# Kernel optimization log

Measured on AMD Instinct MI355X. Metric: run time of the kernel, lower is better.

## Reference

```python
import jax, jax.numpy as jnp
import numpy as np
from jax import lax

NUM_CLASSES = 80
CONF = 0.05
IOU_T = 0.5
K_PER_CLASS = 100   # max_detections_per_class
MAX_DET = 100       # max_detections
BOX_VAR = np.array([0.1, 0.1, 0.2, 0.2], dtype=np.float32)


def make_anchors(H, W):
    """AnchorBox.get_anchors: [x, y, w, h] anchors for strides 8..128."""
    ratios = [0.5, 1.0, 2.0]
    scales = [2.0 ** 0, 2.0 ** (1.0 / 3.0), 2.0 ** (2.0 / 3.0)]
    strides = [8, 16, 32, 64, 128]
    areas = [32.0 ** 2, 64.0 ** 2, 128.0 ** 2, 256.0 ** 2, 512.0 ** 2]
    out = []
    for stride, area in zip(strides, areas):
        fh = int(np.ceil(H / stride)); fw = int(np.ceil(W / stride))
        dims = []
        for r in ratios:
            ah = np.sqrt(area / r); aw = area / ah
            for s in scales:
                dims.append([aw * s, ah * s])
        dims = np.array(dims, dtype=np.float32)              # [9,2]
        rx = (np.arange(fw, dtype=np.float32) + 0.5) * stride
        ry = (np.arange(fh, dtype=np.float32) + 0.5) * stride
        cx, cy = np.meshgrid(rx, ry)                         # [fh,fw]
        centers = np.stack([cx, cy], axis=-1)                # [fh,fw,2]
        centers = np.tile(centers[:, :, None, :], (1, 1, 9, 1))
        d = np.tile(dims[None, None, :, :], (fh, fw, 1, 1))
        out.append(np.concatenate([centers, d], axis=-1).reshape(-1, 4))
    return np.concatenate(out, axis=0).astype(np.float32)   # [N,4]


def _iou_matrix(boxes):
    # boxes: [K,4] corner format (x1,y1,x2,y2)
    lt = jnp.maximum(boxes[:, None, :2], boxes[None, :, :2])
    rb = jnp.minimum(boxes[:, None, 2:], boxes[None, :, 2:])
    inter = jnp.prod(jnp.clip(rb - lt, 0.0), axis=-1)
    area = jnp.prod(boxes[:, 2:] - boxes[:, :2], axis=-1)
    union = area[:, None] + area[None, :] - inter
    return inter / jnp.maximum(union, 1e-8)


def _decode(predictions, anchors):
    box_pred = predictions[..., :4] * jnp.asarray(BOX_VAR)
    xy = box_pred[..., :2] * anchors[:, 2:] + anchors[:, :2]
    wh = jnp.exp(box_pred[..., 2:]) * anchors[:, 2:]
    boxes = jnp.concatenate([xy - wh / 2.0, xy + wh / 2.0], axis=-1)  # [B,N,4] corners
    cls = jax.nn.sigmoid(predictions[..., 4:])                        # [B,N,C]
    return boxes, cls


def _nms_image(boxes, cls_scores):
    # boxes [N,4], cls_scores [N,C]
    rng = jnp.arange(K_PER_CLASS)

    def per_class(scores):  # [N]
        top_s, idx = lax.top_k(scores, K_PER_CLASS)
        cb = boxes[idx]                                      # [K,4]
        iou = lax.stop_gradient(_iou_matrix(cb))
        keep0 = top_s > CONF
        def body(i, keep):
            sup = keep[i] & (iou[i] > IOU_T) & (rng > i)
            return keep & (~sup)
        keep = lax.fori_loop(0, K_PER_CLASS, body, keep0)
        return cb, jnp.where(keep, top_s, -1.0)

    cboxes, cscores = jax.vmap(per_class)(cls_scores.T)      # [C,K,4], [C,K]
    cids = jnp.broadcast_to(jnp.arange(NUM_CLASSES, dtype=jnp.float32)[:, None],
                            (NUM_CLASSES, K_PER_CLASS))
    flat_s = cscores.reshape(-1)
    flat_b = cboxes.reshape(-1, 4)
    flat_c = cids.reshape(-1)
    fs, fi = lax.top_k(flat_s, MAX_DET)
    fb = flat_b[fi]
    fc = flat_c[fi]
    mask = fs > 0.0
    valid = jnp.sum(mask).astype(jnp.int32)
    return (jnp.where(mask[:, None], fb, 0.0),
            jnp.where(mask, fs, 0.0),
            jnp.where(mask, fc, 0.0),
            valid)


def setup_inputs() -> dict:
    key = jax.random.key(0)
    k1, k2 = jax.random.split(key)
    images = jax.random.normal(k1, (8, 512, 512, 3), dtype=jnp.float32)
    predictions = jax.random.normal(k2, (8, 49104, 84), dtype=jnp.float32)
    return {"images": images, "predictions": predictions}


def reference(images, predictions):
    H, W = images.shape[1], images.shape[2]
    anchors = jnp.asarray(make_anchors(H, W))                # [49104,4]
    boxes, cls = _decode(predictions, anchors)
    nmsed_boxes, nmsed_scores, nmsed_classes, valid = jax.vmap(_nms_image)(boxes, cls)
    return nmsed_boxes, nmsed_scores, nmsed_classes, valid
```

## Files before the change

### kernel.cpp

```cpp
#include <hip/hip_runtime.h>
#include <math.h>
#include <stdint.h>

#define NANCH 49104
#define NCLS 80
#define KSEL 100
#define NFLAT (NCLS * KSEL)
#define PREDC 84
#define NB 8
#define ECAP 128
#define BATF4 (NANCH * (PREDC / 4))
#define BPB 256
#define PCAP 16
#define LCAP 16
#define OCAP 64
#define FASTN 512
#define RMAX 8
#define CGRP 5
#define NCHUNK (NCLS / CGRP)
#define THRL 2.5f

struct DimsTable { float d[5][9][2]; };
struct KT { uint32_t key; int tie; };
typedef unsigned long long u64;

__device__ __forceinline__ uint32_t f2key(float f) {
    uint32_t u = __float_as_uint(f);
    return u ^ (uint32_t((int32_t)u >> 31) | 0x80000000u);
}
__device__ __forceinline__ float key2f(uint32_t k) {
    uint32_t u = (k & 0x80000000u) ? (k ^ 0x80000000u) : ~k;
    return __uint_as_float(u);
}
__device__ __forceinline__ float sigm(float x) { return 1.0f / (1.0f + expf(-x)); }

__device__ __forceinline__ void decode_box(const float4 pv, int n,
                                           const DimsTable& dt, float box[4]) {
    int lev, base, fw, stride;
    if (n < 36864)      { lev = 0; base = 0;     fw = 64; stride = 8;   }
    else if (n < 46080) { lev = 1; base = 36864; fw = 32; stride = 16;  }
    else if (n < 48384) { lev = 2; base = 46080; fw = 16; stride = 32;  }
    else if (n < 48960) { lev = 3; base = 48384; fw = 8;  stride = 64;  }
    else                { lev = 4; base = 48960; fw = 4;  stride = 128; }
    int i = n - base;
    int k = i % 9;
    int cell = i / 9;
    int xq = cell % fw, yq = cell / fw;
    float cx = ((float)xq + 0.5f) * (float)stride;
    float cy = ((float)yq + 0.5f) * (float)stride;
    float aw = dt.d[lev][k][0];
    float ah = dt.d[lev][k][1];
    float tx = __fmul_rn(pv.x, 0.1f);
    float ty = __fmul_rn(pv.y, 0.1f);
    float tw = __fmul_rn(pv.z, 0.2f);
    float th = __fmul_rn(pv.w, 0.2f);
    float px = __fadd_rn(__fmul_rn(tx, aw), cx);
    float py = __fadd_rn(__fmul_rn(ty, ah), cy);
    float pw = __fmul_rn(expf(tw), aw);
    float ph = __fmul_rn(expf(th), ah);
    float hw = __fmul_rn(pw, 0.5f);
    float hh = __fmul_rn(ph, 0.5f);
    box[0] = __fsub_rn(px, hw);
    box[1] = __fsub_rn(py, hh);
    box[2] = __fadd_rn(px, hw);
    box[3] = __fadd_rn(py, hh);
}

struct alignas(16) SelSh {
    int hist[2048];
    int suffix[256];
    uint32_t candKey[KSEL];
    int candIdx[KSEL];
    uint32_t eIdx[ECAP];
    uint32_t sKey[KSEL];
    int sIdx[KSEL];
    int cntG, cntE, krem, newkrem, digit, flast, rmin;
    uint32_t prefix, thrKey;
};

template <typename G>
__device__ int block_select(G get, int N, int K, SelSh& sh) {
    const int tid = threadIdx.x;
    int Ksel = (N < K) ? N : K;
    if (Ksel <= 0) return 0;

    if (N <= K) {
        if (tid < N) { KT e = get(tid); sh.candKey[tid] = e.key; sh.candIdx[tid] = e.tie; }
        __syncthreads();
        if (tid < N) {
            uint32_t mk = sh.candKey[tid]; int mi = sh.candIdx[tid];
            int rank = 0;
            for (int j = 0; j < N; ++j) {
                uint32_t kj = sh.candKey[j]; int ij = sh.candIdx[j];
                rank += (kj > mk) || (kj == mk && ij < mi);
            }
            sh.sKey[rank] = mk; sh.sIdx[rank] = mi;
        }
        __syncthreads();
        return Ksel;
    }

    if (tid == 0) { sh.krem = K; sh.prefix = 0; }
    for (int pass = 0; pass < 3; ++pass) {
        const int bins   = (pass == 2) ? 1024 : 2048;
        const int dshift = (pass == 0) ? 21 : (pass == 1 ? 10 : 0);
        const int fshift = (pass == 1) ? 21 : 10;
        const int dmask  = bins - 1;
        for (int j = tid; j < bins; j += 256) sh.hist[j] = 0;
        __syncthreads();
        const uint32_t pref = sh.prefix;
        for (int i = tid; i < N; i += 256) {
            uint32_t key = get(i).key;
            if (pass == 0) {
                atomicAdd(&sh.hist[(key >> dshift) & dmask], 1);
            } else if ((key >> fshift) == pref) {
                atomicAdd(&sh.hist[(key >> dshift) & dmask], 1);
            }
        }
        __syncthreads();
        const int cpb = bins / 256;
        const int base = tid * cpb;
        int lsum = 0;
        for (int j = 0; j < cpb; ++j) lsum += sh.hist[base + j];
        sh.suffix[tid] = lsum;
        __syncthreads();
        for (int off = 1; off < 256; off <<= 1) {
            int v = (tid + off < 256) ? sh.suffix[tid + off] : 0;
            __syncthreads();
            sh.suffix[tid] += v;
            __syncthreads();
        }
        {
            int cum = sh.suffix[tid] - lsum;
            const int krem = sh.krem;
            for (int j = cpb - 1; j >= 0; --j) {
                int cnt = sh.hist[base + j];
                if (cnt > 0 && cum < krem && cum + cnt >= krem) {
                    sh.digit = base + j;
                    sh.newkrem = krem - cum;
                }
                cum += cnt;
            }
        }
        __syncthreads();
        if (tid == 0) {
            sh.krem = sh.newkrem;
            if (pass == 0)      sh.prefix = (uint32_t)sh.digit;
            else if (pass == 1) sh.prefix = (sh.prefix << 11) | (uint32_t)sh.digit;
            else                sh.thrKey = (sh.prefix << 10) | (uint32_t)sh.digit;
        }
        __syncthreads();
    }

    if (tid == 0) { sh.cntG = 0; sh.cntE = 0; }
    __syncthreads();
    const uint32_t thr = sh.thrKey;
    for (int i = tid; i < N; i += 256) {
        KT e = get(i);
        if (e.key > thr) {
            int g = atomicAdd(&sh.cntG, 1);
            sh.candKey[g] = e.key; sh.candIdx[g] = e.tie;
        } else if (e.key == thr) {
            int idx = atomicAdd(&sh.cntE, 1);
            if (idx < ECAP) sh.eIdx[idx] = (uint32_t)e.tie;
        }
    }
    __syncthreads();
    const int need = sh.krem;
    const int nG = K - need;
    if (sh.cntE <= ECAP) {
        const int ce = sh.cntE;
        if (tid < ce) {
            uint32_t my = sh.eIdx[tid];
            int rank = 0;
            for (int j = 0; j < ce; ++j) rank += (sh.eIdx[j] < my);
            if (rank < need) { sh.candKey[nG + rank] = thr; sh.candIdx[nG + rank] = (int)my; }
        }
    } else {
        if (tid == 0) sh.flast = -1;
        __syncthreads();
        for (int t = 0; t < need; ++t) {
            if (tid == 0) sh.rmin = 0x7FFFFFFF;
            __syncthreads();
            const int fl = sh.flast;
            int lmin = 0x7FFFFFFF;
            for (int i = tid; i < N; i += 256) {
                KT e = get(i);
                if (e.key == thr && e.tie > fl) lmin = min(lmin, e.tie);
            }
            atomicMin(&sh.rmin, lmin);
            __syncthreads();
            if (tid == 0) { sh.candKey[nG + t] = thr; sh.candIdx[nG + t] = sh.rmin; sh.flast = sh.rmin; }
            __syncthreads();
        }
    }
    __syncthreads();
    if (tid < K) {
        uint32_t mk = sh.candKey[tid]; int mi = sh.candIdx[tid];
        int rank = 0;
        for (int j = 0; j < K; ++j) {
            uint32_t kj = sh.candKey[j]; int ij = sh.candIdx[j];
            rank += (kj > mk) || (kj == mk && ij < mi);
        }
        sh.sKey[rank] = mk; sh.sIdx[rank] = mi;
    }
    __syncthreads();
    return Ksel;
}

__global__ __launch_bounds__(256) void init_k(int* __restrict__ oflowCnt) {
    for (int x = threadIdx.x; x < NB * NCLS; x += 256) oflowCnt[x] = 0;
}

__device__ __forceinline__ void procf4(float4 p, int v, int b,
                                       int* lcnt, uint2 (*buck)[LCAP],
                                       int* oflowCnt, uint2* oflow) {
    uint32_t q = (uint32_t)v / 21u;
    uint32_t j = (uint32_t)v - q * 21u;
    if (j == 0u) return;
    bool c0 = p.x > THRL, c1 = p.y > THRL, c2 = p.z > THRL, c3 = p.w > THRL;
    if (!(c0 | c1 | c2 | c3)) return;
    uint32_t row = q - (uint32_t)b * (uint32_t)NANCH;
    int cbase = ((int)j - 1) * 4;
    float vv[4] = {p.x, p.y, p.z, p.w};
    bool pp[4] = {c0, c1, c2, c3};
#pragma unroll
    for (int k = 0; k < 4; ++k) {
        if (pp[k]) {
            int c = cbase + k;
            uint32_t key = f2key(sigm(vv[k]));
            int slot = atomicAdd(&lcnt[c], 1);
            if (slot < LCAP) {
                buck[c][slot] = make_uint2(key, row);
            } else {
                int bc = b * NCLS + c;
                int gs = atomicAdd(&oflowCnt[bc], 1);
                if (gs < OCAP) oflow[(size_t)bc * OCAP + gs] = make_uint2(key, row);
            }
        }
    }
}

__global__ __launch_bounds__(256) void cand_scan(const float4* __restrict__ predv,
                                                 uint2* __restrict__ cand2,
                                                 int* __restrict__ cnt2,
                                                 int* __restrict__ oflowCnt,
                                                 uint2* __restrict__ oflow) {
    __shared__ uint2 buck[NCLS][LCAP];
    __shared__ int lcnt[NCLS];

    const int tid = threadIdx.x;
    const int b = blockIdx.x / BPB;
    const int part = blockIdx.x - b * BPB;
    const int CH = (BATF4 + BPB - 1) / BPB;

    for (int j = tid; j < NCLS; j += 256) lcnt[j] = 0;
    __syncthreads();

    int s = b * BATF4 + part * CH;
    int e = b * BATF4 + BATF4;
    if (s + CH < e) e = s + CH;

    int v = s + tid;
    for (; v + 7 * 256 < e; v += 8 * 256) {
        float4 a0 = predv[v];
        float4 a1 = predv[v + 1 * 256];
        float4 a2 = predv[v + 2 * 256];
        float4 a3 = predv[v + 3 * 256];
        float4 a4 = predv[v + 4 * 256];
        float4 a5 = predv[v + 5 * 256];
        float4 a6 = predv[v + 6 * 256];
        float4 a7 = predv[v + 7 * 256];
        procf4(a0, v,           b, lcnt, buck, oflowCnt, oflow);
        procf4(a1, v + 1 * 256, b, lcnt, buck, oflowCnt, oflow);
        procf4(a2, v + 2 * 256, b, lcnt, buck, oflowCnt, oflow);
        procf4(a3, v + 3 * 256, b, lcnt, buck, oflowCnt, oflow);
        procf4(a4, v + 4 * 256, b, lcnt, buck, oflowCnt, oflow);
        procf4(a5, v + 5 * 256, b, lcnt, buck, oflowCnt, oflow);
        procf4(a6, v + 6 * 256, b, lcnt, buck, oflowCnt, oflow);
        procf4(a7, v + 7 * 256, b, lcnt, buck, oflowCnt, oflow);
    }
    for (; v < e; v += 256)
        procf4(predv[v], v, b, lcnt, buck, oflowCnt, oflow);
    __syncthreads();

    if (tid < NCLS) {
        int lc = lcnt[tid];
        if (lc > LCAP) lc = LCAP;
        cnt2[((size_t)b * NCLS + tid) * BPB + part] = lc;
    }
    for (int x = tid; x < NCLS * LCAP; x += 256) {
        int c = x >> 4;
        int k = x & (LCAP - 1);
        int lc = lcnt[c];
        if (lc > LCAP) lc = LCAP;
        if (k < lc)
            cand2[((size_t)(b * NCLS + c) * PCAP + k) * BPB + part] = buck[c][k];
    }
}

__global__ __launch_bounds__(256) void nms_sel(const float* __restrict__ pred,
                                               const uint2* __restrict__ cand2,
                                               const int* __restrict__ cnt2,
                                               const int* __restrict__ oflowCnt,
                                               const uint2* __restrict__ oflow,
                                               float* __restrict__ cls_boxes,
                                               uint32_t* __restrict__ posKeyC,
                                               uint32_t* __restrict__ posFlatC,
                                               int* __restrict__ posCntC,
                                               DimsTable dt) {
    __shared__ SelSh sh;
    __shared__ uint16_t prank[4][FASTN];
    __shared__ int wtot[4];
    __shared__ float sbox[KSEL][4];
    __shared__ float sarea[KSEL];
    __shared__ int sconf[KSEL];
    __shared__ alignas(16) uint32_t sup[KSEL][4];
    __shared__ uint32_t keepm[4];
    const int c = blockIdx.x;
    const int b = blockIdx.y;
    const int tid = threadIdx.x;
    const int bc = b * NCLS + c;
    const int lane = tid & 63;
    const int wid = tid >> 6;

    int myc = cnt2[(size_t)bc * BPB + tid];
    {
        int x = myc;
        for (int off = 1; off < 64; off <<= 1) {
            int y = __shfl_up(x, off);
            if (lane >= off) x += y;
        }
        if (lane == 63) wtot[wid] = x;
        __syncthreads();
        int base = 0;
#pragma unroll
        for (int w = 0; w < 4; ++w) if (w < wid) base += wtot[w];
        sh.suffix[tid] = base + x - myc;
    }
    const int excl = sh.suffix[tid];
    const int n0 = wtot[0] + wtot[1] + wtot[2] + wtot[3];
    const int of = oflowCnt[bc];
    const int n = n0 + of;

    if (n >= KSEL && n <= FASTN && of <= OCAP) {
        u64* list64 = (u64*)sh.hist;
        for (int k = 0; k < myc; ++k) {
            uint2 p = cand2[((size_t)bc * PCAP + k) * BPB + tid];
            list64[excl + k] = ((u64)p.x << 32) | (u64)(~p.y);
        }
        for (int x = tid; x < of; x += 256) {
            uint2 p = oflow[(size_t)bc * OCAP + x];
            list64[n0 + x] = ((u64)p.x << 32) | (u64)(~p.y);
        }
        __syncthreads();
        u64 cl[RMAX];
        int pr[RMAX];
#pragma unroll
        for (int r = 0; r < RMAX; ++r) {
            int i = r * 64 + lane;
            cl[r] = (i < n) ? list64[i] : 0xFFFFFFFFFFFFFFFFull;
            pr[r] = 0;
        }
        const int js = (wid * n) >> 2;
        const int je = ((wid + 1) * n) >> 2;
        int j = js;
        for (; j + 3 < je; j += 4) {
            u64 o0 = list64[j];
            u64 o1 = list64[j + 1];
            u64 o2 = list64[j + 2];
            u64 o3 = list64[j + 3];
#pragma unroll
            for (int r = 0; r < RMAX; ++r)
                pr[r] += (o0 > cl[r]) + (o1 > cl[r]) + (o2 > cl[r]) + (o3 > cl[r]);
        }
        for (; j < je; ++j) {
            u64 o = list64[j];
#pragma unroll
            for (int r = 0; r < RMAX; ++r) pr[r] += (o > cl[r]);
        }
#pragma unroll
        for (int r = 0; r < RMAX; ++r) {
            int i = r * 64 + lane;
            if (i < n) prank[wid][i] = (uint16_t)pr[r];
        }
        __syncthreads();
        for (int i = tid; i < n; i += 256) {
            int rank = (int)prank[0][i] + (int)prank[1][i]
                     + (int)prank[2][i] + (int)prank[3][i];
            if (rank < KSEL) {
                u64 e = list64[i];
                sh.sKey[rank] = (uint32_t)(e >> 32);
                sh.sIdx[rank] = (int)(~(uint32_t)e);
            }
        }
        __syncthreads();
    } else {
        const float* src = pred + (size_t)b * NANCH * PREDC + 4 + c;
        auto g = [src](int i) { KT e; e.key = f2key(sigm(src[(size_t)i * PREDC])); e.tie = i; return e; };
        block_select(g, NANCH, KSEL, sh);
    }

    for (int x = tid; x < KSEL * 4; x += 256) ((uint32_t*)sup)[x] = 0;
    if (tid < KSEL) {
        int ni = sh.sIdx[tid];
        float4 pv = reinterpret_cast<const float4*>(pred)[((size_t)b * NANCH + ni) * (PREDC / 4)];
        float bx[4]; decode_box(pv, ni, dt, bx);
        sbox[tid][0] = bx[0]; sbox[tid][1] = bx[1];
        sbox[tid][2] = bx[2]; sbox[tid][3] = bx[3];
        sarea[tid] = __fmul_rn(__fsub_rn(bx[2], bx[0]), __fsub_rn(bx[3], bx[1]));
        sconf[tid] = (key2f(sh.sKey[tid]) > 0.05f) ? 1 : 0;
    }
    __syncthreads();

    for (int pidx = tid; pidx < KSEL * KSEL; pidx += 256) {
        int i = pidx / KSEL;
        int jj = pidx - i * KSEL;
        if (jj > i && sconf[i] && sconf[jj]) {
            float x1 = fmaxf(sbox[i][0], sbox[jj][0]);
            float y1 = fmaxf(sbox[i][1], sbox[jj][1]);
            float x2 = fminf(sbox[i][2], sbox[jj][2]);
            float y2 = fminf(sbox[i][3], sbox[jj][3]);
            float iw = fmaxf(__fsub_rn(x2, x1), 0.0f);
            float ih = fmaxf(__fsub_rn(y2, y1), 0.0f);
            float inter = __fmul_rn(iw, ih);
            float uni = __fsub_rn(__fadd_rn(sarea[i], sarea[jj]), inter);
            if (__fdiv_rn(inter, fmaxf(uni, 1e-8f)) > 0.5f)
                atomicOr(&sup[i][jj >> 5], 1u << (jj & 31));
        }
    }
    __syncthreads();

    if (tid < 64) {
        const int l = tid;
        uint4 rowA = *reinterpret_cast<const uint4*>(sup[l]);
        int confA = sconf[l];
        uint4 rowB = make_uint4(0u, 0u, 0u, 0u);
        int confB = 0;
        if (l + 64 < KSEL) {
            rowB = *reinterpret_cast<const uint4*>(sup[l + 64]);
            confB = sconf[l + 64];
        }
        u64 mA = __ballot(confA != 0);
        u64 mB = __ballot(confB != 0);
        uint32_t k0 = (uint32_t)mA, k1 = (uint32_t)(mA >> 32);
        uint32_t k2 = (uint32_t)mB, k3 = (uint32_t)(mB >> 32);
        for (int i = 0; i < KSEL; ++i) {
            uint32_t w = (i < 32) ? k0 : (i < 64) ? k1 : (i < 96) ? k2 : k3;
            if ((w >> (i & 31)) & 1u) {
                uint32_t s0, s1, s2, s3;
                if (i < 64) {
                    s0 = __shfl(rowA.x, i); s1 = __shfl(rowA.y, i);
                    s2 = __shfl(rowA.z, i); s3 = __shfl(rowA.w, i);
                } else {
                    s0 = __shfl(rowB.x, i - 64); s1 = __shfl(rowB.y, i - 64);
                    s2 = __shfl(rowB.z, i - 64); s3 = __shfl(rowB.w, i - 64);
                }
                k0 &= ~s0; k1 &= ~s1; k2 &= ~s2; k3 &= ~s3;
            }
        }
        if (l == 0) {
            keepm[0] = k0; keepm[1] = k1; keepm[2] = k2; keepm[3] = k3;
            posCntC[bc] = __popc(k0) + __popc(k1) + __popc(k2) + __popc(k3);
        }
    }
    __syncthreads();

    if (tid < KSEL) {
        reinterpret_cast<float4*>(cls_boxes)[(size_t)b * NFLAT + c * KSEL + tid] =
            make_float4(sbox[tid][0], sbox[tid][1], sbox[tid][2], sbox[tid][3]);
        int w = tid >> 5, bit = tid & 31;
        if ((keepm[w] >> bit) & 1u) {
            int off = __popc(keepm[w] & ((bit == 0) ? 0u : ((1u << bit) - 1u)));
            for (int ww = 0; ww < w; ++ww) off += __popc(keepm[ww]);
            posKeyC[(size_t)bc * KSEL + off] = sh.sKey[tid];
            posFlatC[(size_t)bc * KSEL + off] = (uint32_t)(c * KSEL + tid);
        }
    }
}

__global__ __launch_bounds__(256) void chunk_sel(const uint32_t* __restrict__ posKeyC,
                                                 const uint32_t* __restrict__ posFlatC,
                                                 const int* __restrict__ posCntC,
                                                 u64* __restrict__ chunkOut,
                                                 int* __restrict__ chunkN) {
    __shared__ u64 list64[FASTN];
    __shared__ uint16_t prank[4][FASTN];
    __shared__ int csh[CGRP + 1];
    __shared__ u64 osel[KSEL];
    const int g = blockIdx.x;
    const int b = blockIdx.y;
    const int tid = threadIdx.x;
    const int lane = tid & 63;
    const int wid = tid >> 6;
    const int c0 = g * CGRP;

    if (tid == 0) {
        int acc = 0;
        for (int cc = 0; cc < CGRP; ++cc) {
            csh[cc] = acc;
            acc += posCntC[b * NCLS + c0 + cc];
        }
        csh[CGRP] = acc;
    }
    __syncthreads();
    const int n = csh[CGRP];

    for (int idx = tid; idx < CGRP * KSEL; idx += 256) {
        int cc = idx / KSEL;
        int k = idx - cc * KSEL;
        int base = csh[cc];
        if (k < csh[cc + 1] - base) {
            size_t sp = (size_t)(b * NCLS + c0 + cc) * KSEL + k;
            list64[base + k] = ((u64)posKeyC[sp] << 32) | (u64)(~posFlatC[sp]);
        }
    }
    __syncthreads();

    if (n > 0) {
        u64 cl[RMAX];
        int pr[RMAX];
#pragma unroll
        for (int r = 0; r < RMAX; ++r) {
            int i = r * 64 + lane;
            cl[r] = (i < n) ? list64[i] : 0xFFFFFFFFFFFFFFFFull;
            pr[r] = 0;
        }
        const int js = (wid * n) >> 2;
        const int je = ((wid + 1) * n) >> 2;
        int j = js;
        for (; j + 3 < je; j += 4) {
            u64 o0 = list64[j];
            u64 o1 = list64[j + 1];
            u64 o2 = list64[j + 2];
            u64 o3 = list64[j + 3];
#pragma unroll
            for (int r = 0; r < RMAX; ++r)
                pr[r] += (o0 > cl[r]) + (o1 > cl[r]) + (o2 > cl[r]) + (o3 > cl[r]);
        }
        for (; j < je; ++j) {
            u64 o = list64[j];
#pragma unroll
            for (int r = 0; r < RMAX; ++r) pr[r] += (o > cl[r]);
        }
#pragma unroll
        for (int r = 0; r < RMAX; ++r) {
            int i = r * 64 + lane;
            if (i < n) prank[wid][i] = (uint16_t)pr[r];
        }
        __syncthreads();
        for (int i = tid; i < n; i += 256) {
            int rank = (int)prank[0][i] + (int)prank[1][i]
                     + (int)prank[2][i] + (int)prank[3][i];
            if (rank < KSEL) osel[rank] = list64[i];
        }
    }
    __syncthreads();
    const int kn = (n < KSEL) ? n : KSEL;
    if (tid < kn)
        chunkOut[(size_t)(b * NCHUNK + g) * KSEL + tid] = osel[tid];
    if (tid == 0) chunkN[b * NCHUNK + g] = kn;
}

__global__ __launch_bounds__(256) void merge_sel(const u64* __restrict__ chunkOut,
                                                 const int* __restrict__ chunkN,
                                                 const float* __restrict__ cls_boxes,
                                                 float* __restrict__ out) {
    __shared__ u64 lst[NCHUNK][KSEL];
    __shared__ int ln[NCHUNK];
    __shared__ u64 osel[KSEL];
    __shared__ int okcnt;
    const int b = blockIdx.x;
    const int tid = threadIdx.x;

    if (tid < NCHUNK) ln[tid] = chunkN[b * NCHUNK + tid];
    if (tid == 0) okcnt = 0;
    __syncthreads();
    for (int x = tid; x < NCHUNK * KSEL; x += 256) {
        int g = x / KSEL;
        int k = x - g * KSEL;
        lst[g][k] = (k < ln[g]) ? chunkOut[(size_t)(b * NCHUNK + g) * KSEL + k] : 0ull;
    }
    __syncthreads();

    if (tid < 64) {
        const int l = tid;
        u64 h = (l < NCHUNK) ? lst[l][0] : 0ull;
        int p = 0;
        for (int r = 0; r < KSEL; ++r) {
            u64 m = h;
#pragma unroll
            for (int off = 8; off >= 1; off >>= 1) {
                u64 o = __shfl_xor(m, off);
                if (o > m) m = o;
            }
            if (l < NCHUNK && h == m && m != 0ull) {
                ++p;
                h = (p < ln[l]) ? lst[l][p] : 0ull;
            }
            if (l == 0) osel[r] = m;
        }
    }
    __syncthreads();

    if (tid < KSEL) {
        u64 e = osel[tid];
        float4 ob = make_float4(0.f, 0.f, 0.f, 0.f);
        float sv = 0.f, cv = 0.f;
        if (e != 0ull) {
            uint32_t key = (uint32_t)(e >> 32);
            int flat = (int)(~(uint32_t)e);
            sv = key2f(key);
            ob = reinterpret_cast<const float4*>(cls_boxes)[(size_t)b * NFLAT + flat];
            cv = (float)(flat / KSEL);
            atomicAdd(&okcnt, 1);
        }
        reinterpret_cast<float4*>(out)[(size_t)b * KSEL + tid] = ob;
        out[NB * KSEL * 4 + b * KSEL + tid] = sv;
        out[NB * KSEL * 5 + b * KSEL + tid] = cv;
    }
    __syncthreads();
    if (tid == 0) out[NB * KSEL * 6 + b] = (float)okcnt;
}

extern "C" void kernel_launch(void* const* d_in, const int* in_sizes, int n_in,
                              void* d_out, int out_size, void* d_ws, size_t ws_size,
                              hipStream_t stream) {
    const float* pred = (const float*)d_in[1];
    float* out = (float*)d_out;

    DimsTable dt;
    const double areasd[5] = {1024.0, 4096.0, 16384.0, 65536.0, 262144.0};
    const double ratios[3] = {0.5, 1.0, 2.0};
    const double scales[3] = {1.0, pow(2.0, 1.0 / 3.0), pow(2.0, 2.0 / 3.0)};
    for (int l = 0; l < 5; ++l)
        for (int ri = 0; ri < 3; ++ri) {
            double ah = sqrt(areasd[l] / ratios[ri]);
            double aw = areasd[l] / ah;
            for (int si = 0; si < 3; ++si) {
                dt.d[l][ri * 3 + si][0] = (float)(aw * scales[si]);
                dt.d[l][ri * 3 + si][1] = (float)(ah * scales[si]);
            }
        }

    char* wsb = (char*)d_ws;
    int* oflowCnt = (int*)wsb;
    int* posCntC  = oflowCnt + NB * NCLS;
    int* chunkNb  = posCntC + NB * NCLS;
    uint2* oflow  = (uint2*)(wsb + 16384);
    uint2* cand2  = oflow + (size_t)NB * NCLS * OCAP;
    int* cnt2     = (int*)(cand2 + (size_t)NB * NCLS * PCAP * BPB);
    float* cls_boxes = (float*)(cnt2 + (size_t)NB * NCLS * BPB);
    uint32_t* posKeyC  = (uint32_t*)(cls_boxes + (size_t)NB * NFLAT * 4);
    uint32_t* posFlatC = posKeyC + (size_t)NB * NFLAT;
    u64* chunkOut = (u64*)(posFlatC + (size_t)NB * NFLAT);

    init_k<<<1, 256, 0, stream>>>(oflowCnt);

    cand_scan<<<NB * BPB, 256, 0, stream>>>(reinterpret_cast<const float4*>(pred),
                                            cand2, cnt2, oflowCnt, oflow);

    dim3 gb(NCLS, NB);
    nms_sel<<<gb, 256, 0, stream>>>(pred, cand2, cnt2, oflowCnt, oflow,
                                    cls_boxes, posKeyC, posFlatC, posCntC, dt);

    dim3 gc(NCHUNK, NB);
    chunk_sel<<<gc, 256, 0, stream>>>(posKeyC, posFlatC, posCntC, chunkOut, chunkNb);

    merge_sel<<<NB, 256, 0, stream>>>(chunkOut, chunkNb, cls_boxes, out);
}
```

Baseline: 118.5 us.

## Fuse chunk selection and merge into a single two-level k-way merge kernel

Replaces the two-kernel top-K pipeline (per-chunk rank-based selection over 16 chunks of 5 classes, then a 16-way merge) with one kernel per image. Each of four wavefronts runs a 20-way heap-head merge over sorted per-class lists using 32-lane shuffles, and a second 4-way merge then picks the final top 100. This removes a kernel launch and the chunkOut round trip through global memory. In exchange, each image is handled by a single block running two serial 100-step merge loops, with 64 KB of shared memory for the lists.

Result: slower. 143.6 us (+21.2%).

```diff
diff --git a/kernel.cpp b/kernel.cpp
--- a/kernel.cpp
+++ b/kernel.cpp
@@ -16,8 +16,6 @@
 #define OCAP 64
 #define FASTN 512
 #define RMAX 8
-#define CGRP 5
-#define NCHUNK (NCLS / CGRP)
 #define THRL 2.5f
 
 struct DimsTable { float d[5][9][2]; };
@@ -479,126 +477,70 @@
     }
 }
 
-__global__ __launch_bounds__(256) void chunk_sel(const uint32_t* __restrict__ posKeyC,
-                                                 const uint32_t* __restrict__ posFlatC,
-                                                 const int* __restrict__ posCntC,
-                                                 u64* __restrict__ chunkOut,
-                                                 int* __restrict__ chunkN) {
-    __shared__ u64 list64[FASTN];
-    __shared__ uint16_t prank[4][FASTN];
-    __shared__ int csh[CGRP + 1];
-    __shared__ u64 osel[KSEL];
-    const int g = blockIdx.x;
-    const int b = blockIdx.y;
-    const int tid = threadIdx.x;
-    const int lane = tid & 63;
-    const int wid = tid >> 6;
-    const int c0 = g * CGRP;
-
-    if (tid == 0) {
-        int acc = 0;
-        for (int cc = 0; cc < CGRP; ++cc) {
-            csh[cc] = acc;
-            acc += posCntC[b * NCLS + c0 + cc];
-        }
-        csh[CGRP] = acc;
-    }
-    __syncthreads();
-    const int n = csh[CGRP];
-
-    for (int idx = tid; idx < CGRP * KSEL; idx += 256) {
-        int cc = idx / KSEL;
-        int k = idx - cc * KSEL;
-        int base = csh[cc];
-        if (k < csh[cc + 1] - base) {
-            size_t sp = (size_t)(b * NCLS + c0 + cc) * KSEL + k;
-            list64[base + k] = ((u64)posKeyC[sp] << 32) | (u64)(~posFlatC[sp]);
-        }
-    }
-    __syncthreads();
-
-    if (n > 0) {
-        u64 cl[RMAX];
-        int pr[RMAX];
-#pragma unroll
-        for (int r = 0; r < RMAX; ++r) {
-            int i = r * 64 + lane;
-            cl[r] = (i < n) ? list64[i] : 0xFFFFFFFFFFFFFFFFull;
-            pr[r] = 0;
-        }
-        const int js = (wid * n) >> 2;
-        const int je = ((wid + 1) * n) >> 2;
-        int j = js;
-        for (; j + 3 < je; j += 4) {
-            u64 o0 = list64[j];
-            u64 o1 = list64[j + 1];
-            u64 o2 = list64[j + 2];
-            u64 o3 = list64[j + 3];
-#pragma unroll
-            for (int r = 0; r < RMAX; ++r)
-                pr[r] += (o0 > cl[r]) + (o1 > cl[r]) + (o2 > cl[r]) + (o3 > cl[r]);
-        }
-        for (; j < je; ++j) {
-            u64 o = list64[j];
-#pragma unroll
-            for (int r = 0; r < RMAX; ++r) pr[r] += (o > cl[r]);
-        }
-#pragma unroll
-        for (int r = 0; r < RMAX; ++r) {
-            int i = r * 64 + lane;
-            if (i < n) prank[wid][i] = (uint16_t)pr[r];
-        }
-        __syncthreads();
-        for (int i = tid; i < n; i += 256) {
-            int rank = (int)prank[0][i] + (int)prank[1][i]
-                     + (int)prank[2][i] + (int)prank[3][i];
-            if (rank < KSEL) osel[rank] = list64[i];
-        }
-    }
-    __syncthreads();
-    const int kn = (n < KSEL) ? n : KSEL;
-    if (tid < kn)
-        chunkOut[(size_t)(b * NCHUNK + g) * KSEL + tid] = osel[tid];
-    if (tid == 0) chunkN[b * NCHUNK + g] = kn;
-}
-
-__global__ __launch_bounds__(256) void merge_sel(const u64* __restrict__ chunkOut,
-                                                 const int* __restrict__ chunkN,
-                                                 const float* __restrict__ cls_boxes,
-                                                 float* __restrict__ out) {
-    __shared__ u64 lst[NCHUNK][KSEL];
-    __shared__ int ln[NCHUNK];
+__global__ __launch_bounds__(256) void final_merge(const uint32_t* __restrict__ posKeyC,
+                                                   const uint32_t* __restrict__ posFlatC,
+                                                   const int* __restrict__ posCntC,
+                                                   const float* __restrict__ cls_boxes,
+                                                   float* __restrict__ out) {
+    __shared__ u64 lst[NCLS][KSEL];
+    __shared__ int ln[NCLS];
+    __shared__ u64 mid[4][KSEL];
     __shared__ u64 osel[KSEL];
     __shared__ int okcnt;
     const int b = blockIdx.x;
     const int tid = threadIdx.x;
-
-    if (tid < NCHUNK) ln[tid] = chunkN[b * NCHUNK + tid];
+    const int lane = tid & 63;
+    const int wid = tid >> 6;
+
+    if (tid < NCLS) ln[tid] = posCntC[b * NCLS + tid];
     if (tid == 0) okcnt = 0;
     __syncthreads();
-    for (int x = tid; x < NCHUNK * KSEL; x += 256) {
-        int g = x / KSEL;
-        int k = x - g * KSEL;
-        lst[g][k] = (k < ln[g]) ? chunkOut[(size_t)(b * NCHUNK + g) * KSEL + k] : 0ull;
-    }
-    __syncthreads();
-
-    if (tid < 64) {
-        const int l = tid;
-        u64 h = (l < NCHUNK) ? lst[l][0] : 0ull;
+    for (int x = tid; x < NCLS * KSEL; x += 256) {
+        int c = x / KSEL;
+        int k = x - c * KSEL;
+        size_t sp = (size_t)(b * NCLS + c) * KSEL + k;
+        lst[c][k] = (k < ln[c]) ? (((u64)posKeyC[sp] << 32) | (u64)(~posFlatC[sp]))
+                                : 0ull;
+    }
+    __syncthreads();
+
+    {
+        const int c = wid * 20 + lane;
+        u64 h = (lane < 20 && ln[c] > 0) ? lst[c][0] : 0ull;
         int p = 0;
         for (int r = 0; r < KSEL; ++r) {
             u64 m = h;
 #pragma unroll
-            for (int off = 8; off >= 1; off >>= 1) {
-                u64 o = __shfl_xor(m, off);
+            for (int off = 16; off >= 1; off >>= 1) {
+                u64 o = __shfl_xor(m, off, 32);
                 if (o > m) m = o;
             }
-            if (l < NCHUNK && h == m && m != 0ull) {
+            m = __shfl(m, 0);
+            if (lane < 20 && h == m && m != 0ull) {
                 ++p;
-                h = (p < ln[l]) ? lst[l][p] : 0ull;
-            }
-            if (l == 0) osel[r] = m;
+                h = (p < ln[c]) ? lst[c][p] : 0ull;
+            }
+            if (lane == 0) mid[wid][r] = m;
+        }
+    }
+    __syncthreads();
+
+    if (wid == 0) {
+        u64 h = (lane < 4) ? mid[lane][0] : 0ull;
+        int p = 0;
+        for (int r = 0; r < KSEL; ++r) {
+            u64 m = h;
+#pragma unroll
+            for (int off = 2; off >= 1; off >>= 1) {
+                u64 o = __shfl_xor(m, off, 4);
+                if (o > m) m = o;
+            }
+            m = __shfl(m, 0);
+            if (lane < 4 && h == m && m != 0ull) {
+                ++p;
+                h = (p < KSEL) ? mid[lane][p] : 0ull;
+            }
+            if (lane == 0) osel[r] = m;
         }
     }
     __syncthreads();
@@ -646,14 +588,12 @@
     char* wsb = (char*)d_ws;
     int* oflowCnt = (int*)wsb;
     int* posCntC  = oflowCnt + NB * NCLS;
-    int* chunkNb  = posCntC + NB * NCLS;
     uint2* oflow  = (uint2*)(wsb + 16384);
     uint2* cand2  = oflow + (size_t)NB * NCLS * OCAP;
     int* cnt2     = (int*)(cand2 + (size_t)NB * NCLS * PCAP * BPB);
     float* cls_boxes = (float*)(cnt2 + (size_t)NB * NCLS * BPB);
     uint32_t* posKeyC  = (uint32_t*)(cls_boxes + (size_t)NB * NFLAT * 4);
     uint32_t* posFlatC = posKeyC + (size_t)NB * NFLAT;
-    u64* chunkOut = (u64*)(posFlatC + (size_t)NB * NFLAT);
 
     init_k<<<1, 256, 0, stream>>>(oflowCnt);
 
@@ -664,8 +604,5 @@
     nms_sel<<<gb, 256, 0, stream>>>(pred, cand2, cnt2, oflowCnt, oflow,
                                     cls_boxes, posKeyC, posFlatC, posCntC, dt);
 
-    dim3 gc(NCHUNK, NB);
-    chunk_sel<<<gc, 256, 0, stream>>>(posKeyC, posFlatC, posCntC, chunkOut, chunkNb);
-
-    merge_sel<<<NB, 256, 0, stream>>>(chunkOut, chunkNb, cls_boxes, out);
-}
+    final_merge<<<NB, 256, 0, stream>>>(posKeyC, posFlatC, posCntC, cls_boxes, out);
+}
```
